# Kernel optimization log

Measured on AMD Instinct MI355X. Metric: run time of the kernel, lower is better.

Reference implementation:

```python
import jax, jax.numpy as jnp
import numpy as np

INPUT_SIZE = 512
HIDDEN = 1024
OUT = 4
SEQ = 2048


def setup_inputs() -> dict:
    key = jax.random.key(0)
    ks = jax.random.split(key, 12)
    s_in = 1.0 / np.sqrt(INPUT_SIZE)
    s_h = 1.0 / np.sqrt(HIDDEN)
    inp = {
        "x": jax.random.normal(ks[0], (SEQ, INPUT_SIZE), jnp.float32),
        "h0": jnp.zeros((1, 1, HIDDEN), jnp.float32),
        "c0": jnp.zeros((1, 1, HIDDEN), jnp.float32),
        # LSTM params (PyTorch layout: gates ordered i, f, g, o along 4H)
        "w_ih": jax.random.uniform(ks[1], (4 * HIDDEN, INPUT_SIZE), jnp.float32, -s_h, s_h),
        "w_hh": jax.random.uniform(ks[2], (4 * HIDDEN, HIDDEN), jnp.float32, -s_h, s_h),
        "b_ih": jax.random.uniform(ks[3], (4 * HIDDEN,), jnp.float32, -s_h, s_h),
        "b_hh": jax.random.uniform(ks[4], (4 * HIDDEN,), jnp.float32, -s_h, s_h),
        "fc1_w": jax.random.uniform(ks[5], (HIDDEN, HIDDEN), jnp.float32, -s_h, s_h),
        "fc1_b": jax.random.uniform(ks[6], (HIDDEN,), jnp.float32, -s_h, s_h),
        "fc2_w": jax.random.uniform(ks[7], (HIDDEN, HIDDEN), jnp.float32, -s_h, s_h),
        "fc2_b": jax.random.uniform(ks[8], (HIDDEN,), jnp.float32, -s_h, s_h),
        "mean_w": jax.random.uniform(ks[9], (OUT, HIDDEN), jnp.float32, -s_h, s_h),
        "mean_b": jax.random.uniform(ks[10], (OUT,), jnp.float32, -s_h, s_h),
        "log_std": jnp.zeros((OUT,), jnp.float32),
    }
    return inp


def _lstm(x, h0, c0, w_ih, w_hh, b_ih, b_hh):
    # Precompute input projections for all timesteps: [T, 4H]
    gx = x @ w_ih.T + b_ih + b_hh
    H = h0.shape[-1]

    def step(carry, gx_t):
        h, c = carry  # [H], [H]
        g = gx_t + h @ w_hh.T  # [4H]
        i = jax.nn.sigmoid(g[0 * H:1 * H])
        f = jax.nn.sigmoid(g[1 * H:2 * H])
        gg = jnp.tanh(g[2 * H:3 * H])
        o = jax.nn.sigmoid(g[3 * H:4 * H])
        c_new = f * c + i * gg
        h_new = o * jnp.tanh(c_new)
        return (h_new, c_new), h_new

    (hT, cT), ys = jax.lax.scan(step, (h0[0, 0], c0[0, 0]), gx)
    return ys, hT[None, None, :], cT[None, None, :]  # ys: [T, H]


def reference(x, h0, c0, w_ih, w_hh, b_ih, b_hh, fc1_w, fc1_b, fc2_w, fc2_b, mean_w, mean_b, log_std):
    ys, hT, cT = _lstm(x, h0, c0, w_ih, w_hh, b_ih, b_hh)
    h1 = jax.nn.relu(ys @ fc1_w.T + fc1_b)
    h2 = jax.nn.relu(h1 @ fc2_w.T + fc2_b)
    action_mean = h2 @ mean_w.T + mean_b  # [T, OUT]
    action_log_std = jnp.broadcast_to(log_std, action_mean.shape)
    return action_mean, action_log_std, hT, cT
```

## Files before the change

kernel.cpp:

```cpp
#include <hip/hip_runtime.h>
#include <stdint.h>


#define T_SEQ 2048
#define H 1024
#define G4 4096
#define K_IN 512
#define SENT 0x7FC0DEADu
#define NREP 2
#define RSTRIDE ((T_SEQ + 1) * H)

__device__ __forceinline__ float sigmoidf_(float x) { return 1.0f / (1.0f + __expf(-x)); }
__device__ __forceinline__ float tanhf_(float x) { return 1.0f - 2.0f / (1.0f + __expf(2.0f * x)); }

__device__ __forceinline__ uint4 poll_load16(const uint4* p) {
  uint4 v;
  asm volatile("global_load_dwordx4 %0, %1, off sc0 sc1\n\ts_waitcnt vmcnt(0)"
               : "=v"(v) : "v"(p) : "memory");
  return v;
}

__global__ void init_k(const float* __restrict__ h0, float* __restrict__ h_hist) {
  int idx = blockIdx.x * blockDim.x + threadIdx.x;
  if (idx >= NREP * RSTRIDE) return;
  int k = idx % RSTRIDE;
  if (k < H) {
    h_hist[idx] = h0[k];
  } else {
    ((unsigned*)h_hist)[idx] = SENT;
  }
}

#define BM 64
#define BN 64
#define BK 32
#define LDT 68

template <bool RELU, bool HASB2>
__global__ __launch_bounds__(256) void gemm_bias_k(
    const float* __restrict__ A, const float* __restrict__ Bw,
    const float* __restrict__ b1, const float* __restrict__ b2,
    float* __restrict__ C, int M, int N, int K) {
  __shared__ float As[BK][LDT];
  __shared__ float Bs[BK][LDT];
  const int tid = threadIdx.x;
  const int m0 = blockIdx.y * BM;
  const int n0 = blockIdx.x * BN;
  const int tx = tid & 15, ty = tid >> 4;
  const int srow = tid >> 2;
  const int skq = tid & 3;

  float acc[4][4];
#pragma unroll
  for (int i = 0; i < 4; i++)
#pragma unroll
    for (int j = 0; j < 4; j++) acc[i][j] = 0.f;

  const float* Arow = A + (size_t)(m0 + srow) * K;
  const float* Brow = Bw + (size_t)(n0 + srow) * K;

  for (int k0 = 0; k0 < K; k0 += BK) {
    float4 a0 = *(const float4*)(Arow + k0 + skq * 8);
    float4 a1 = *(const float4*)(Arow + k0 + skq * 8 + 4);
    float4 c0_ = *(const float4*)(Brow + k0 + skq * 8);
    float4 c1_ = *(const float4*)(Brow + k0 + skq * 8 + 4);
    __syncthreads();
    const int kb = skq * 8;
    As[kb + 0][srow] = a0.x; As[kb + 1][srow] = a0.y; As[kb + 2][srow] = a0.z; As[kb + 3][srow] = a0.w;
    As[kb + 4][srow] = a1.x; As[kb + 5][srow] = a1.y; As[kb + 6][srow] = a1.z; As[kb + 7][srow] = a1.w;
    Bs[kb + 0][srow] = c0_.x; Bs[kb + 1][srow] = c0_.y; Bs[kb + 2][srow] = c0_.z; Bs[kb + 3][srow] = c0_.w;
    Bs[kb + 4][srow] = c1_.x; Bs[kb + 5][srow] = c1_.y; Bs[kb + 6][srow] = c1_.z; Bs[kb + 7][srow] = c1_.w;
    __syncthreads();
#pragma unroll
    for (int kk = 0; kk < BK; kk++) {
      float av[4], bv[4];
      *(float4*)av = *(const float4*)&As[kk][ty * 4];
      *(float4*)bv = *(const float4*)&Bs[kk][tx * 4];
#pragma unroll
      for (int i = 0; i < 4; i++)
#pragma unroll
        for (int j = 0; j < 4; j++) acc[i][j] = fmaf(av[i], bv[j], acc[i][j]);
    }
  }

  float bb[4];
#pragma unroll
  for (int j = 0; j < 4; j++) {
    bb[j] = b1[n0 + tx * 4 + j];
    if (HASB2) bb[j] += b2[n0 + tx * 4 + j];
  }
#pragma unroll
  for (int i = 0; i < 4; i++) {
    float4 o;
    float* op = (float*)&o;
#pragma unroll
    for (int j = 0; j < 4; j++) {
      float v = acc[i][j] + bb[j];
      op[j] = RELU ? fmaxf(v, 0.f) : v;
    }
    *(float4*)&C[(size_t)(m0 + ty * 4 + i) * N + n0 + tx * 4] = o;
  }
}

#define NWG 128
#define NTHR 512
#define HPAD 68

#define PIN4(V) asm volatile("" : "+v"((V).x), "+v"((V).y), "+v"((V).z), "+v"((V).w))

__global__ __attribute__((amdgpu_waves_per_eu(2, 2))) __launch_bounds__(NTHR)
void lstm_k(
    const float* __restrict__ gx, const float* __restrict__ w_hh,
    const float* __restrict__ c0, float* __restrict__ h_hist,
    float* __restrict__ out) {
  unsigned* h_u = (unsigned*)h_hist;
  __shared__ float hbuf[2][16 * HPAD];
  const int tid = threadIdx.x;
  const int wg = blockIdx.x;
  const int wave = tid >> 6, lane = tid & 63;
  const int g = lane & 3;
  const int s = lane >> 2;
  const int unit = wg * 8 + wave;
  const int grow = g * 1024 + unit;

  const float* wp = w_hh + (size_t)grow * H + s * 64;
  float4 w0 = *(const float4*)(wp + 0),  w1 = *(const float4*)(wp + 4);
  float4 w2 = *(const float4*)(wp + 8),  w3 = *(const float4*)(wp + 12);
  float4 w4 = *(const float4*)(wp + 16), w5 = *(const float4*)(wp + 20);
  float4 w6 = *(const float4*)(wp + 24), w7 = *(const float4*)(wp + 28);
  float4 w8 = *(const float4*)(wp + 32), w9 = *(const float4*)(wp + 36);
  float4 wA = *(const float4*)(wp + 40), wB = *(const float4*)(wp + 44);
  float4 wC = *(const float4*)(wp + 48), wD = *(const float4*)(wp + 52);
  float4 wE = *(const float4*)(wp + 56), wF = *(const float4*)(wp + 60);
  PIN4(w0); PIN4(w1); PIN4(w2); PIN4(w3);
  PIN4(w4); PIN4(w5); PIN4(w6); PIN4(w7);
  PIN4(w8); PIN4(w9); PIN4(wA); PIN4(wB);
  PIN4(wC); PIN4(wD); PIN4(wE); PIN4(wF);

  float c = c0[unit];

  const bool poller = tid < 256;
  const int stage_idx = 4 * tid + (tid >> 4) * 4;
  unsigned* poll_base = h_u + (size_t)(wg & 1) * RSTRIDE;

  for (int t = 0; t < T_SEQ; t++) {
    const int buf = t & 1;
    float gxv = gx[(size_t)t * G4 + grow];
    asm volatile("" : "+v"(gxv));

    if (poller) {
      const uint4* src = (const uint4*)(poll_base + (size_t)t * H) + tid;
      uint4 v = poll_load16(src);
      while (v.x == SENT || v.y == SENT || v.z == SENT || v.w == SENT)
        v = poll_load16(src);
      float4 f;
      f.x = __uint_as_float(v.x); f.y = __uint_as_float(v.y);
      f.z = __uint_as_float(v.z); f.w = __uint_as_float(v.w);
      *(float4*)&hbuf[buf][stage_idx] = f;
    }
    __syncthreads();

    float acc0 = 0.f, acc1 = 0.f, acc2 = 0.f, acc3 = 0.f;
    const float* hs = &hbuf[buf][s * HPAD];
#define MAC(J, WV)                                  \
  {                                                 \
    float4 hv = *(const float4*)(hs + (J) * 4);     \
    acc0 = fmaf((WV).x, hv.x, acc0);                \
    acc1 = fmaf((WV).y, hv.y, acc1);                \
    acc2 = fmaf((WV).z, hv.z, acc2);                \
    acc3 = fmaf((WV).w, hv.w, acc3);                \
  }
    MAC(0, w0) MAC(1, w1) MAC(2, w2) MAC(3, w3)
    MAC(4, w4) MAC(5, w5) MAC(6, w6) MAC(7, w7)
    MAC(8, w8) MAC(9, w9) MAC(10, wA) MAC(11, wB)
    MAC(12, wC) MAC(13, wD) MAC(14, wE) MAC(15, wF)
#undef MAC
    float accv = (acc0 + acc1) + (acc2 + acc3);
    accv += __shfl_xor(accv, 4);
    accv += __shfl_xor(accv, 8);
    accv += __shfl_xor(accv, 16);
    accv += __shfl_xor(accv, 32);
    float pre = accv + gxv;
    float act = (g == 2) ? tanhf_(pre) : sigmoidf_(pre);
    float b1v = __shfl_xor(act, 1);
    float b2v = __shfl_xor(act, 2);
    float b3v = __shfl_xor(act, 3);
    c = fmaf(b1v, c, act * b2v);
    float hn = b3v * tanhf_(c);
    if (g == 0 && s < NREP) {
      __hip_atomic_store(&h_u[(size_t)s * RSTRIDE + (size_t)(t + 1) * H + unit],
                         __float_as_uint(hn), __ATOMIC_RELAXED,
                         __HIP_MEMORY_SCOPE_AGENT);
      if (t == T_SEQ - 1 && s == 0) {
        out[16384 + unit] = hn;
        out[17408 + unit] = c;
      }
    }
  }
}

__global__ __launch_bounds__(256) void head_k(
    const float* __restrict__ h2, const float* __restrict__ mean_w,
    const float* __restrict__ mean_b, const float* __restrict__ log_std,
    float* __restrict__ out) {
  const int t = blockIdx.x;
  const int tid = threadIdx.x;
  const int wave = tid >> 6, lane = tid & 63;
  const float* hr = h2 + (size_t)t * H;
  const float* wr = mean_w + (size_t)wave * H;
  float s = 0.f;
#pragma unroll
  for (int j = 0; j < 16; j++) s = fmaf(hr[lane + j * 64], wr[lane + j * 64], s);
#pragma unroll
  for (int off = 32; off > 0; off >>= 1) s += __shfl_down(s, off);
  if (lane == 0) out[t * 4 + wave] = s + mean_b[wave];
  if (tid < 4) out[8192 + t * 4 + tid] = log_std[tid];
}

extern "C" void kernel_launch(void* const* d_in, const int* in_sizes, int n_in,
                              void* d_out, int out_size, void* d_ws, size_t ws_size,
                              hipStream_t stream) {
  const float* x      = (const float*)d_in[0];
  const float* h0     = (const float*)d_in[1];
  const float* c0     = (const float*)d_in[2];
  const float* w_ih   = (const float*)d_in[3];
  const float* w_hh   = (const float*)d_in[4];
  const float* b_ih   = (const float*)d_in[5];
  const float* b_hh   = (const float*)d_in[6];
  const float* fc1_w  = (const float*)d_in[7];
  const float* fc1_b  = (const float*)d_in[8];
  const float* fc2_w  = (const float*)d_in[9];
  const float* fc2_b  = (const float*)d_in[10];
  const float* mean_w = (const float*)d_in[11];
  const float* mean_b = (const float*)d_in[12];
  const float* lstd   = (const float*)d_in[13];
  float* out = (float*)d_out;

  float* gx = (float*)d_ws;
  float* h_hist = gx + (size_t)T_SEQ * G4;
  float* h1 = gx;
  float* h2 = gx + (size_t)T_SEQ * H;

  init_k<<<dim3((NREP * RSTRIDE + 255) / 256), 256, 0, stream>>>(h0, h_hist);
  gemm_bias_k<false, true><<<dim3(G4 / BN, T_SEQ / BM), 256, 0, stream>>>(
      x, w_ih, b_ih, b_hh, gx, T_SEQ, G4, K_IN);
  lstm_k<<<dim3(NWG), NTHR, 0, stream>>>(gx, w_hh, c0, h_hist, out);
  gemm_bias_k<true, false><<<dim3(H / BN, T_SEQ / BM), 256, 0, stream>>>(
      h_hist + H, fc1_w, fc1_b, nullptr, h1, T_SEQ, H, H);
  gemm_bias_k<true, false><<<dim3(H / BN, T_SEQ / BM), 256, 0, stream>>>(
      h1, fc2_w, fc2_b, nullptr, h2, T_SEQ, H, H);
  head_k<<<dim3(T_SEQ), 256, 0, stream>>>(h2, mean_w, mean_b, lstd, out);
}
```

Measured before the change: 3.837 ms.

## Poll hidden state per-wave directly from global memory, dropping LDS staging and barriers

```diff
diff --git a/kernel.cpp b/kernel.cpp
--- a/kernel.cpp
+++ b/kernel.cpp
@@ -12,13 +12,6 @@
 
 __device__ __forceinline__ float sigmoidf_(float x) { return 1.0f / (1.0f + __expf(-x)); }
 __device__ __forceinline__ float tanhf_(float x) { return 1.0f - 2.0f / (1.0f + __expf(2.0f * x)); }
-
-__device__ __forceinline__ uint4 poll_load16(const uint4* p) {
-  uint4 v;
-  asm volatile("global_load_dwordx4 %0, %1, off sc0 sc1\n\ts_waitcnt vmcnt(0)"
-               : "=v"(v) : "v"(p) : "memory");
-  return v;
-}
 
 __global__ void init_k(const float* __restrict__ h0, float* __restrict__ h_hist) {
   int idx = blockIdx.x * blockDim.x + threadIdx.x;
@@ -102,9 +95,8 @@
   }
 }
 
-#define NWG 128
-#define NTHR 512
-#define HPAD 68
+#define NWG 256
+#define NTHR 256
 
 #define PIN4(V) asm volatile("" : "+v"((V).x), "+v"((V).y), "+v"((V).z), "+v"((V).w))
 
@@ -114,84 +106,89 @@
     const float* __restrict__ c0, float* __restrict__ h_hist,
     float* __restrict__ out) {
   unsigned* h_u = (unsigned*)h_hist;
-  __shared__ float hbuf[2][16 * HPAD];
   const int tid = threadIdx.x;
-  const int wg = blockIdx.x;
   const int wave = tid >> 6, lane = tid & 63;
-  const int g = lane & 3;
-  const int s = lane >> 2;
-  const int unit = wg * 8 + wave;
-  const int grow = g * 1024 + unit;
-
-  const float* wp = w_hh + (size_t)grow * H + s * 64;
-  float4 w0 = *(const float4*)(wp + 0),  w1 = *(const float4*)(wp + 4);
-  float4 w2 = *(const float4*)(wp + 8),  w3 = *(const float4*)(wp + 12);
-  float4 w4 = *(const float4*)(wp + 16), w5 = *(const float4*)(wp + 20);
-  float4 w6 = *(const float4*)(wp + 24), w7 = *(const float4*)(wp + 28);
-  float4 w8 = *(const float4*)(wp + 32), w9 = *(const float4*)(wp + 36);
-  float4 wA = *(const float4*)(wp + 40), wB = *(const float4*)(wp + 44);
-  float4 wC = *(const float4*)(wp + 48), wD = *(const float4*)(wp + 52);
-  float4 wE = *(const float4*)(wp + 56), wF = *(const float4*)(wp + 60);
-  PIN4(w0); PIN4(w1); PIN4(w2); PIN4(w3);
-  PIN4(w4); PIN4(w5); PIN4(w6); PIN4(w7);
-  PIN4(w8); PIN4(w9); PIN4(wA); PIN4(wB);
-  PIN4(wC); PIN4(wD); PIN4(wE); PIN4(wF);
+  const int unit = blockIdx.x * 4 + wave;
+
+  const size_t cb = (size_t)lane * 16;
+  const float* wpi = w_hh + ((size_t)(0 * 1024 + unit)) * H + cb;
+  const float* wpf = w_hh + ((size_t)(1 * 1024 + unit)) * H + cb;
+  const float* wpg = w_hh + ((size_t)(2 * 1024 + unit)) * H + cb;
+  const float* wpo = w_hh + ((size_t)(3 * 1024 + unit)) * H + cb;
+  float4 wi0 = *(const float4*)(wpi + 0),  wi1 = *(const float4*)(wpi + 4);
+  float4 wi2 = *(const float4*)(wpi + 8),  wi3 = *(const float4*)(wpi + 12);
+  float4 wf0 = *(const float4*)(wpf + 0),  wf1 = *(const float4*)(wpf + 4);
+  float4 wf2 = *(const float4*)(wpf + 8),  wf3 = *(const float4*)(wpf + 12);
+  float4 wg0 = *(const float4*)(wpg + 0),  wg1 = *(const float4*)(wpg + 4);
+  float4 wg2 = *(const float4*)(wpg + 8),  wg3 = *(const float4*)(wpg + 12);
+  float4 wo0 = *(const float4*)(wpo + 0),  wo1 = *(const float4*)(wpo + 4);
+  float4 wo2 = *(const float4*)(wpo + 8),  wo3 = *(const float4*)(wpo + 12);
+  PIN4(wi0); PIN4(wi1); PIN4(wi2); PIN4(wi3);
+  PIN4(wf0); PIN4(wf1); PIN4(wf2); PIN4(wf3);
+  PIN4(wg0); PIN4(wg1); PIN4(wg2); PIN4(wg3);
+  PIN4(wo0); PIN4(wo1); PIN4(wo2); PIN4(wo3);
 
   float c = c0[unit];
-
-  const bool poller = tid < 256;
-  const int stage_idx = 4 * tid + (tid >> 4) * 4;
-  unsigned* poll_base = h_u + (size_t)(wg & 1) * RSTRIDE;
+  const unsigned* poll_rep = h_u + (size_t)(unit & 1) * RSTRIDE;
 
   for (int t = 0; t < T_SEQ; t++) {
-    const int buf = t & 1;
-    float gxv = gx[(size_t)t * G4 + grow];
-    asm volatile("" : "+v"(gxv));
-
-    if (poller) {
-      const uint4* src = (const uint4*)(poll_base + (size_t)t * H) + tid;
-      uint4 v = poll_load16(src);
-      while (v.x == SENT || v.y == SENT || v.z == SENT || v.w == SENT)
-        v = poll_load16(src);
-      float4 f;
-      f.x = __uint_as_float(v.x); f.y = __uint_as_float(v.y);
-      f.z = __uint_as_float(v.z); f.w = __uint_as_float(v.w);
-      *(float4*)&hbuf[buf][stage_idx] = f;
-    }
-    __syncthreads();
-
-    float acc0 = 0.f, acc1 = 0.f, acc2 = 0.f, acc3 = 0.f;
-    const float* hs = &hbuf[buf][s * HPAD];
-#define MAC(J, WV)                                  \
-  {                                                 \
-    float4 hv = *(const float4*)(hs + (J) * 4);     \
-    acc0 = fmaf((WV).x, hv.x, acc0);                \
-    acc1 = fmaf((WV).y, hv.y, acc1);                \
-    acc2 = fmaf((WV).z, hv.z, acc2);                \
-    acc3 = fmaf((WV).w, hv.w, acc3);                \
-  }
-    MAC(0, w0) MAC(1, w1) MAC(2, w2) MAC(3, w3)
-    MAC(4, w4) MAC(5, w5) MAC(6, w6) MAC(7, w7)
-    MAC(8, w8) MAC(9, w9) MAC(10, wA) MAC(11, wB)
-    MAC(12, wC) MAC(13, wD) MAC(14, wE) MAC(15, wF)
-#undef MAC
-    float accv = (acc0 + acc1) + (acc2 + acc3);
-    accv += __shfl_xor(accv, 4);
-    accv += __shfl_xor(accv, 8);
-    accv += __shfl_xor(accv, 16);
-    accv += __shfl_xor(accv, 32);
-    float pre = accv + gxv;
-    float act = (g == 2) ? tanhf_(pre) : sigmoidf_(pre);
-    float b1v = __shfl_xor(act, 1);
-    float b2v = __shfl_xor(act, 2);
-    float b3v = __shfl_xor(act, 3);
-    c = fmaf(b1v, c, act * b2v);
-    float hn = b3v * tanhf_(c);
-    if (g == 0 && s < NREP) {
-      __hip_atomic_store(&h_u[(size_t)s * RSTRIDE + (size_t)(t + 1) * H + unit],
+    const uint4* hb = (const uint4*)(poll_rep + (size_t)t * H) + lane * 4;
+    uint4 p0, p1, p2, p3;
+    for (;;) {
+      asm volatile(
+          "global_load_dwordx4 %0, %4, off sc0 sc1\n\t"
+          "global_load_dwordx4 %1, %4, off offset:16 sc0 sc1\n\t"
+          "global_load_dwordx4 %2, %4, off offset:32 sc0 sc1\n\t"
+          "global_load_dwordx4 %3, %4, off offset:48 sc0 sc1\n\t"
+          "s_waitcnt vmcnt(0)"
+          : "=v"(p0), "=v"(p1), "=v"(p2), "=v"(p3)
+          : "v"(hb) : "memory");
+      unsigned m = p0.x ^ SENT;
+      m = min(m, p0.y ^ SENT); m = min(m, p0.z ^ SENT); m = min(m, p0.w ^ SENT);
+      m = min(m, p1.x ^ SENT); m = min(m, p1.y ^ SENT); m = min(m, p1.z ^ SENT);
+      m = min(m, p1.w ^ SENT); m = min(m, p2.x ^ SENT); m = min(m, p2.y ^ SENT);
+      m = min(m, p2.z ^ SENT); m = min(m, p2.w ^ SENT); m = min(m, p3.x ^ SENT);
+      m = min(m, p3.y ^ SENT); m = min(m, p3.z ^ SENT); m = min(m, p3.w ^ SENT);
+      if (m != 0) break;
+    }
+    const float* gxr = gx + (size_t)t * G4 + unit;
+    float gxi = gxr[0], gxf = gxr[1024], gxg = gxr[2048], gxo = gxr[3072];
+
+    float4 h0f = *(float4*)&p0, h1f = *(float4*)&p1;
+    float4 h2f = *(float4*)&p2, h3f = *(float4*)&p3;
+    float acci = 0.f, accf = 0.f, accg = 0.f, acco = 0.f;
+#define DOT16(W0, W1, W2, W3, ACC)                                   \
+  ACC = fmaf((W0).x, h0f.x, ACC); ACC = fmaf((W0).y, h0f.y, ACC);    \
+  ACC = fmaf((W0).z, h0f.z, ACC); ACC = fmaf((W0).w, h0f.w, ACC);    \
+  ACC = fmaf((W1).x, h1f.x, ACC); ACC = fmaf((W1).y, h1f.y, ACC);    \
+  ACC = fmaf((W1).z, h1f.z, ACC); ACC = fmaf((W1).w, h1f.w, ACC);    \
+  ACC = fmaf((W2).x, h2f.x, ACC); ACC = fmaf((W2).y, h2f.y, ACC);    \
+  ACC = fmaf((W2).z, h2f.z, ACC); ACC = fmaf((W2).w, h2f.w, ACC);    \
+  ACC = fmaf((W3).x, h3f.x, ACC); ACC = fmaf((W3).y, h3f.y, ACC);    \
+  ACC = fmaf((W3).z, h3f.z, ACC); ACC = fmaf((W3).w, h3f.w, ACC);
+    DOT16(wi0, wi1, wi2, wi3, acci)
+    DOT16(wf0, wf1, wf2, wf3, accf)
+    DOT16(wg0, wg1, wg2, wg3, accg)
+    DOT16(wo0, wo1, wo2, wo3, acco)
+#undef DOT16
+#pragma unroll
+    for (int off = 1; off < 64; off <<= 1) {
+      acci += __shfl_xor(acci, off);
+      accf += __shfl_xor(accf, off);
+      accg += __shfl_xor(accg, off);
+      acco += __shfl_xor(acco, off);
+    }
+    float iv = sigmoidf_(acci + gxi);
+    float fv = sigmoidf_(accf + gxf);
+    float gv = tanhf_(accg + gxg);
+    float ov = sigmoidf_(acco + gxo);
+    c = fmaf(fv, c, iv * gv);
+    float hn = ov * tanhf_(c);
+    if (lane < NREP) {
+      __hip_atomic_store(&h_u[(size_t)lane * RSTRIDE + (size_t)(t + 1) * H + unit],
                          __float_as_uint(hn), __ATOMIC_RELAXED,
                          __HIP_MEMORY_SCOPE_AGENT);
-      if (t == T_SEQ - 1 && s == 0) {
+      if (t == T_SEQ - 1 && lane == 0) {
         out[16384 + unit] = hn;
         out[17408 + unit] = c;
       }
```

Measured after the change: 10.57 ms. 175% more time.
